# Kernel optimization log

Hardware: AMD Instinct MI355X
Metric: run time of the kernel (lower is better)

Reference implementation:

```python
import jax, jax.numpy as jnp
import numpy as np


def _lap(cost):
    """Jonker-Volgenant / e-maxx O(n^3) Hungarian (min-cost) on a square
    float64 cost matrix. Returns col index assigned to each row, matching
    scipy.optimize.linear_sum_assignment for square inputs.
    Inner column scan is vectorized with numpy.
    """
    n = cost.shape[0]
    INF = np.inf
    C = np.zeros((n + 1, n + 1), dtype=np.float64)
    C[1:, 1:] = cost  # 1-indexed
    u = np.zeros(n + 1)
    v = np.zeros(n + 1)
    p = np.zeros(n + 1, dtype=np.int64)    # p[j] = row matched to col j
    way = np.zeros(n + 1, dtype=np.int64)
    for i in range(1, n + 1):
        p[0] = i
        j0 = 0
        minv = np.full(n + 1, INF)
        used = np.zeros(n + 1, dtype=bool)
        while True:
            used[j0] = True
            i0 = p[j0]
            free = ~used
            free[0] = False
            cur = C[i0] - u[i0] - v
            upd = free & (cur < minv)
            minv = np.where(upd, cur, minv)
            way[upd] = j0
            mv = np.where(free, minv, INF)
            j1 = int(np.argmin(mv))
            delta = mv[j1]
            u[p[used]] += delta
            v[used] -= delta
            minv = np.where(free, minv - delta, minv)
            j0 = j1
            if p[j0] == 0:
                break
        # augment along alternating path
        while j0 != 0:
            j1 = way[j0]
            p[j0] = p[j1]
            j0 = j1
    col_for_row = np.zeros(n, dtype=np.int64)
    col_for_row[p[1:] - 1] = np.arange(n)
    return col_for_row


def _match(D_np):
    """Per-sample min-max normalize (detached) then Hungarian match."""
    B, N, _ = D_np.shape
    cols = np.zeros((B, N), dtype=np.int64)
    for b in range(B):
        Db = D_np[b]
        d_min = Db.min()
        d_range = Db.max() - d_min + 1e-8
        cols[b] = _lap((Db - d_min) / d_range)
    return cols


def setup_inputs() -> dict:
    key = jax.random.key(0)
    B, N = 32, 512
    D = jax.random.uniform(key, (B, N, N), dtype=jnp.float32)
    return {"D": D}


def reference(D):
    B, N, _ = D.shape
    # Matching indices are computed on detached, normalized costs (CPU, like
    # the original .cpu().numpy() round-trip).
    D_np = np.asarray(jax.device_get(D), dtype=np.float64)
    cols = jnp.asarray(_match(D_np))                      # [B, N]
    bi = jnp.arange(B)[:, None]
    ri = jnp.arange(N)[None, :]
    matched = D[bi, ri, cols]                             # [B, N], original D
    return matched.mean(axis=1).mean()
```

## Files before the change

### kernel.cpp

```cpp
#include <hip/hip_runtime.h>
#include <hip/hip_fp16.h>


#define NN 512
#define LPT 8
#define BIGF 1e30f
#define QCAP 2080
#define ARRCAP 1536

#define DPP_MINF(x, CTRL) do {                                                  \
    float _t = __int_as_float(__builtin_amdgcn_update_dpp(                      \
        __float_as_int(x), __float_as_int(x), CTRL, 0xf, 0xf, false));          \
    (x) = _t < (x) ? _t : (x);                                                  \
} while (0)

__device__ __forceinline__ float wave_min_f32(float x) {
    DPP_MINF(x, 0x111);
    DPP_MINF(x, 0x112);
    DPP_MINF(x, 0x114);
    DPP_MINF(x, 0x118);
    DPP_MINF(x, 0x142);
    DPP_MINF(x, 0x143);
    return __int_as_float(__builtin_amdgcn_readlane(__float_as_int(x), 63));
}

template <bool F16>
__global__ __launch_bounds__(64)
void hungarian_kernel(const float* __restrict__ D, const __half* __restrict__ Hm,
                      double* __restrict__ bsum) {
    const int b    = blockIdx.x;
    const int lane = threadIdx.x;
    const float*  __restrict__ Db = D + (size_t)b * NN * NN;
    const __half* __restrict__ Hb = F16 ? (Hm + (size_t)b * NN * NN) : (const __half*)nullptr;

    __shared__ int p[NN + 1];
    __shared__ int way[NN + 1];
    __shared__ int xrow[NN + 1];
    __shared__ int q[QCAP];
    __shared__ int qn[2];

    for (int k = lane; k <= NN; k += 64) { p[k] = 0; way[k] = 0; xrow[k] = 0; }
    __syncthreads();

    const int col0 = lane * LPT;

    auto loadrow = [&](int r, float rv[LPT]) {
        if constexpr (F16) {
            const uint4 qv = *(const uint4*)(Hb + (size_t)(r - 1) * NN + col0);
            __half2 h0 = *(__half2*)&qv.x, h1 = *(__half2*)&qv.y,
                    h2 = *(__half2*)&qv.z, h3 = *(__half2*)&qv.w;
            float2 f0 = __half22float2(h0), f1 = __half22float2(h1),
                   f2 = __half22float2(h2), f3 = __half22float2(h3);
            rv[0]=f0.x; rv[1]=f0.y; rv[2]=f1.x; rv[3]=f1.y;
            rv[4]=f2.x; rv[5]=f2.y; rv[6]=f3.x; rv[7]=f3.y;
        } else {
            const float4* rp = (const float4*)(Db + (size_t)(r - 1) * NN + col0);
            const float4 a = rp[0], c = rp[1];
            rv[0]=a.x; rv[1]=a.y; rv[2]=a.z; rv[3]=a.w;
            rv[4]=c.x; rv[5]=c.y; rv[6]=c.z; rv[7]=c.w;
        }
    };
    auto loadsc = [&](int r, int j) -> float {
        if constexpr (F16) return __half2float(Hb[(size_t)(r - 1) * NN + (j - 1)]);
        else               return Db[(size_t)(r - 1) * NN + (j - 1)];
    };

    float v[LPT];

    {
        float cmin[LPT]; int cidx[LPT];
        #pragma unroll
        for (int s = 0; s < LPT; ++s) { cmin[s] = BIGF; cidx[s] = 0; }
        for (int r = 1; r <= NN; ++r) {
            float rv[LPT]; loadrow(r, rv);
            #pragma unroll
            for (int s = 0; s < LPT; ++s) {
                if (rv[s] < cmin[s]) { cmin[s] = rv[s]; cidx[s] = r; }
            }
        }
        #pragma unroll
        for (int s = 0; s < LPT; ++s) { v[s] = cmin[s]; way[col0 + s + 1] = cidx[s]; }
        __syncthreads();
        if (lane == 0) {
            for (int j = NN; j >= 1; --j) {
                const int i = way[j];
                if (xrow[i] == 0) { xrow[i] = j; p[j] = i; }
            }
        }
        __syncthreads();
    }

    if (lane == 0) {
        int t = 0;
        for (int r = 1; r <= NN; ++r) if (xrow[r] == 0) q[t++] = r;
        qn[0] = t;
    }
    __syncthreads();
    {
        int tail = qn[0], head = 0, processed = 0;
        while (head < tail && processed < ARRCAP) {
            const int i = q[head]; ++head; ++processed;
            float rv[LPT]; loadrow(i, rv);
            float cur[LPT];
            #pragma unroll
            for (int s = 0; s < LPT; ++s) cur[s] = rv[s] - v[s];
            float b1 = BIGF; int bj = NN;
            #pragma unroll
            for (int s = 0; s < LPT; ++s) {
                if (cur[s] < b1) { b1 = cur[s]; bj = col0 + s + 1; }
            }
            const float u1 = wave_min_f32(b1);
            const unsigned long long m1 = __ballot(b1 == u1);
            const int owner = __ffsll(m1) - 1;
            const int j1    = __builtin_amdgcn_readlane(bj, owner);
            const int slotU = (j1 - 1) & 7;
            #pragma unroll
            for (int s = 0; s < LPT; ++s)
                if (lane == owner && s == slotU) cur[s] = BIGF;
            float b2 = BIGF;
            #pragma unroll
            for (int s = 0; s < LPT; ++s) b2 = cur[s] < b2 ? cur[s] : b2;
            const float u2 = wave_min_f32(b2);

            const int i1 = p[j1];
            const bool steal = (u1 < u2);
            if (steal && lane == owner) {
                #pragma unroll
                for (int s = 0; s < LPT; ++s) if (s == slotU) v[s] -= (u2 - u1);
            }
            if (i1 == 0) {
                if (lane == 0) { p[j1] = i; xrow[i] = j1; }
            } else if (steal && tail < QCAP - 1) {
                if (lane == 0) { p[j1] = i; xrow[i] = j1; xrow[i1] = 0; q[tail] = i1; }
                ++tail;
            }
            __syncthreads();
        }
    }
    __syncthreads();

    if (lane == 0) {
        int t = 0;
        for (int r = 1; r <= NN; ++r) if (xrow[r] == 0) q[t++] = r;
        qn[0] = t;
    }
    __syncthreads();
    const int nfree = qn[0];

    for (int fi = 0; fi < nfree; ++fi) {
        const int i = q[fi];
        if (lane == 0) p[0] = i;

        float minv[LPT]; int wayreg[LPT];
        #pragma unroll
        for (int s = 0; s < LPT; ++s) { minv[s] = BIGF; wayreg[s] = 0; }
        unsigned usedmask = 0;
        int   j0 = 0;
        float uu = 0.0f;

        float rv[LPT]; loadrow(i, rv);
        __syncthreads();

        float dfinal;
        while (true) {
            if (j0 > 0) {
                const int jc = j0 - 1;
                if ((jc >> 3) == lane) usedmask |= 1u << (jc & 7);
            }
            float bestv = BIGF; int bestj = NN;
            #pragma unroll
            for (int s = 0; s < LPT; ++s) {
                const bool freeS = !(usedmask & (1u << s));
                const float cur  = rv[s] - uu - v[s];
                const bool upd   = freeS && (cur < minv[s]);
                minv[s]   = upd ? cur : minv[s];
                wayreg[s] = upd ? j0  : wayreg[s];
                const bool better = freeS && (minv[s] < bestv);
                bestj = better ? (col0 + s + 1) : bestj;
                bestv = better ? minv[s] : bestv;
            }
            const float dmin = wave_min_f32(bestv);
            const unsigned long long mk = __ballot(bestv == dmin);
            const int owner = __ffsll(mk) - 1;
            const int j1    = __builtin_amdgcn_readlane(bestj, owner);

            const int i0n = p[j1];
            if (i0n == 0) { j0 = j1; dfinal = dmin; break; }

            const int slotU = (j1 - 1) & 7;
            float vs = v[0];
            #pragma unroll
            for (int s = 1; s < LPT; ++s) vs = (slotU == s) ? v[s] : vs;
            const float vj1 = __int_as_float(
                __builtin_amdgcn_readlane(__float_as_int(vs), owner));

            const float csc = loadsc(i0n, j1);
            loadrow(i0n, rv);
            uu = csc - vj1 - dmin;
            j0 = j1;
        }

        #pragma unroll
        for (int s = 0; s < LPT; ++s) {
            way[col0 + s + 1] = wayreg[s];
            if (usedmask & (1u << s)) v[s] += minv[s] - dfinal;
        }
        __syncthreads();
        if (lane == 0) {
            int jj = j0;
            while (jj != 0) { const int jp = way[jj]; p[jj] = p[jp]; jj = jp; }
        }
        __syncthreads();
    }

    double acc = 0.0;
    #pragma unroll
    for (int s = 0; s < LPT; ++s) {
        const int j = col0 + s + 1;
        const int r = p[j] - 1;
        acc += (double)Db[(size_t)r * NN + (j - 1)];
    }
    #pragma unroll
    for (int m = 1; m < 64; m <<= 1) acc += __shfl_xor(acc, m, 64);
    if (lane == 0) bsum[b] = acc;
}

__global__ void cvt_kernel(const float* __restrict__ D, __half* __restrict__ H, int n4) {
    const int idx = blockIdx.x * blockDim.x + threadIdx.x;
    const int stride = gridDim.x * blockDim.x;
    const float4* __restrict__ D4 = (const float4*)D;
    __half2* __restrict__ H2 = (__half2*)H;
    for (int i = idx; i < n4; i += stride) {
        const float4 f = D4[i];
        H2[2 * i]     = __floats2half2_rn(f.x, f.y);
        H2[2 * i + 1] = __floats2half2_rn(f.z, f.w);
    }
}

__global__ void finalize_kernel(const double* __restrict__ bsum, float* __restrict__ out, int B) {
    if (threadIdx.x == 0 && blockIdx.x == 0) {
        double acc = 0.0;
        for (int b = 0; b < B; ++b) acc += bsum[b] / (double)NN;
        out[0] = (float)(acc / (double)B);
    }
}

extern "C" void kernel_launch(void* const* d_in, const int* in_sizes, int n_in,
                              void* d_out, int out_size, void* d_ws, size_t ws_size,
                              hipStream_t stream) {
    (void)n_in; (void)out_size;
    const float* D    = (const float*)d_in[0];
    float*       out  = (float*)d_out;
    double*      bsum = (double*)d_ws;

    const int B = in_sizes[0] / (NN * NN);
    const size_t need = 256 + (size_t)B * NN * NN * sizeof(__half);

    if (ws_size >= need) {
        __half* Hm = (__half*)((char*)d_ws + 256);
        const int n4 = (B * NN * NN) / 4;
        cvt_kernel<<<1024, 256, 0, stream>>>(D, Hm, n4);
        hungarian_kernel<true><<<dim3(B), dim3(64), 0, stream>>>(D, Hm, bsum);
    } else {
        hungarian_kernel<false><<<dim3(B), dim3(64), 0, stream>>>(D, nullptr, bsum);
    }
    finalize_kernel<<<1, 64, 0, stream>>>(bsum, out, B);
}
```

Baseline: 2.956 ms.

## Keep assignment in registers, add reduction-transfer pass, replace barriers with wave barriers

Mirrors the column-to-row assignment array into per-lane registers so the augmenting loops read it via readlane instead of shared memory. Adds a JV reduction-transfer pass before the auction-style augmenting row reduction. Replaces the used bitmask with an additive blocking array and precomputed row-minus-v values, and uses tree argmin helpers. Swaps __syncthreads for wave barriers since the block is a single wave. The extra pass adds work and changes the heuristic's path, which could alter the number of Dijkstra searches.

```diff
diff --git a/kernel.cpp b/kernel.cpp
--- a/kernel.cpp
+++ b/kernel.cpp
@@ -24,6 +24,30 @@
     return __int_as_float(__builtin_amdgcn_readlane(__float_as_int(x), 63));
 }
 
+__device__ __forceinline__ void wavebar() { __builtin_amdgcn_wave_barrier(); }
+
+__device__ __forceinline__ int sel8i(const int a[LPT], int slot) {
+    int r = a[0];
+    #pragma unroll
+    for (int s = 1; s < LPT; ++s) r = (slot == s) ? a[s] : r;
+    return r;
+}
+__device__ __forceinline__ float sel8f(const float a[LPT], int slot) {
+    float r = a[0];
+    #pragma unroll
+    for (int s = 1; s < LPT; ++s) r = (slot == s) ? a[s] : r;
+    return r;
+}
+__device__ __forceinline__ void argmin8(const float e[LPT], float& bv, int& bs) {
+    float v01 = e[1] < e[0] ? e[1] : e[0]; int s01 = e[1] < e[0] ? 1 : 0;
+    float v23 = e[3] < e[2] ? e[3] : e[2]; int s23 = e[3] < e[2] ? 3 : 2;
+    float v45 = e[5] < e[4] ? e[5] : e[4]; int s45 = e[5] < e[4] ? 5 : 4;
+    float v67 = e[7] < e[6] ? e[7] : e[6]; int s67 = e[7] < e[6] ? 7 : 6;
+    float v03 = v23 < v01 ? v23 : v01;     int s03 = v23 < v01 ? s23 : s01;
+    float v47 = v67 < v45 ? v67 : v45;     int s47 = v67 < v45 ? s67 : s45;
+    bv = v47 < v03 ? v47 : v03;            bs = v47 < v03 ? s47 : s03;
+}
+
 template <bool F16>
 __global__ __launch_bounds__(64)
 void hungarian_kernel(const float* __restrict__ D, const __half* __restrict__ Hm,
@@ -33,14 +57,14 @@
     const float*  __restrict__ Db = D + (size_t)b * NN * NN;
     const __half* __restrict__ Hb = F16 ? (Hm + (size_t)b * NN * NN) : (const __half*)nullptr;
 
-    __shared__ int p[NN + 1];
-    __shared__ int way[NN + 1];
-    __shared__ int xrow[NN + 1];
+    __shared__ __align__(16) int pc[NN];
+    __shared__ __align__(16) int wayc[NN];
+    __shared__ __align__(16) int xrowc[NN];
     __shared__ int q[QCAP];
-    __shared__ int qn[2];
-
-    for (int k = lane; k <= NN; k += 64) { p[k] = 0; way[k] = 0; xrow[k] = 0; }
-    __syncthreads();
+    __shared__ int qn;
+
+    for (int k = lane; k < NN; k += 64) { pc[k] = 0; wayc[k] = 0; xrowc[k] = 0; }
+    wavebar();
 
     const int col0 = lane * LPT;
 
@@ -66,159 +90,201 @@
     };
 
     float v[LPT];
+    int   preg[LPT];
 
     {
         float cmin[LPT]; int cidx[LPT];
         #pragma unroll
         for (int s = 0; s < LPT; ++s) { cmin[s] = BIGF; cidx[s] = 0; }
+        #pragma unroll 4
         for (int r = 1; r <= NN; ++r) {
             float rv[LPT]; loadrow(r, rv);
             #pragma unroll
             for (int s = 0; s < LPT; ++s) {
-                if (rv[s] < cmin[s]) { cmin[s] = rv[s]; cidx[s] = r; }
-            }
-        }
-        #pragma unroll
-        for (int s = 0; s < LPT; ++s) { v[s] = cmin[s]; way[col0 + s + 1] = cidx[s]; }
-        __syncthreads();
+                const bool c = rv[s] < cmin[s];
+                cidx[s] = c ? r : cidx[s];
+                cmin[s] = c ? rv[s] : cmin[s];
+            }
+        }
+        #pragma unroll
+        for (int s = 0; s < LPT; ++s) v[s] = cmin[s];
+        *(int4*)&wayc[col0]     = make_int4(cidx[0], cidx[1], cidx[2], cidx[3]);
+        *(int4*)&wayc[col0 + 4] = make_int4(cidx[4], cidx[5], cidx[6], cidx[7]);
+        wavebar();
         if (lane == 0) {
             for (int j = NN; j >= 1; --j) {
-                const int i = way[j];
-                if (xrow[i] == 0) { xrow[i] = j; p[j] = i; }
-            }
-        }
-        __syncthreads();
+                const int i = wayc[j - 1];
+                if (xrowc[i - 1] == 0) { xrowc[i - 1] = j; pc[j - 1] = i; }
+            }
+        }
+        wavebar();
+        const int4 p0 = *(const int4*)&pc[col0];
+        const int4 p1 = *(const int4*)&pc[col0 + 4];
+        preg[0]=p0.x; preg[1]=p0.y; preg[2]=p0.z; preg[3]=p0.w;
+        preg[4]=p1.x; preg[5]=p1.y; preg[6]=p1.z; preg[7]=p1.w;
+    }
+
+    int xr[LPT];
+    {
+        const int4 x0 = *(const int4*)&xrowc[col0];
+        const int4 x1 = *(const int4*)&xrowc[col0 + 4];
+        xr[0]=x0.x; xr[1]=x0.y; xr[2]=x0.z; xr[3]=x0.w;
+        xr[4]=x1.x; xr[5]=x1.y; xr[6]=x1.z; xr[7]=x1.w;
+    }
+
+    for (int i = 1; i <= NN; ++i) {
+        const int jx = __builtin_amdgcn_readlane(sel8i(xr, (i - 1) & 7), (i - 1) >> 3);
+        if (jx == 0) continue;
+        float rv[LPT]; loadrow(i, rv);
+        const int  ow = (jx - 1) >> 3, sl = (jx - 1) & 7;
+        const bool am = (lane == ow);
+        float lm = BIGF;
+        #pragma unroll
+        for (int s = 0; s < LPT; ++s) {
+            const float t = (am && s == sl) ? BIGF : (rv[s] - v[s]);
+            lm = t < lm ? t : lm;
+        }
+        const float mu = wave_min_f32(lm);
+        #pragma unroll
+        for (int s = 0; s < LPT; ++s)
+            if (am && s == sl) v[s] = rv[s] - mu;
     }
 
     if (lane == 0) {
         int t = 0;
-        for (int r = 1; r <= NN; ++r) if (xrow[r] == 0) q[t++] = r;
-        qn[0] = t;
-    }
-    __syncthreads();
+        for (int r = 1; r <= NN; ++r) if (xrowc[r - 1] == 0) q[t++] = r;
+        qn = t;
+    }
+    wavebar();
     {
-        int tail = qn[0], head = 0, processed = 0;
+        int tail = qn, head = 0, processed = 0;
         while (head < tail && processed < ARRCAP) {
             const int i = q[head]; ++head; ++processed;
             float rv[LPT]; loadrow(i, rv);
             float cur[LPT];
             #pragma unroll
             for (int s = 0; s < LPT; ++s) cur[s] = rv[s] - v[s];
-            float b1 = BIGF; int bj = NN;
-            #pragma unroll
-            for (int s = 0; s < LPT; ++s) {
-                if (cur[s] < b1) { b1 = cur[s]; bj = col0 + s + 1; }
-            }
+            float b1; int bs1; argmin8(cur, b1, bs1);
             const float u1 = wave_min_f32(b1);
             const unsigned long long m1 = __ballot(b1 == u1);
             const int owner = __ffsll(m1) - 1;
-            const int j1    = __builtin_amdgcn_readlane(bj, owner);
+            const int j1    = __builtin_amdgcn_readlane(col0 + bs1 + 1, owner);
             const int slotU = (j1 - 1) & 7;
+            const bool am   = (lane == owner);
             #pragma unroll
             for (int s = 0; s < LPT; ++s)
-                if (lane == owner && s == slotU) cur[s] = BIGF;
+                if (am && s == slotU) cur[s] = BIGF;
             float b2 = BIGF;
             #pragma unroll
             for (int s = 0; s < LPT; ++s) b2 = cur[s] < b2 ? cur[s] : b2;
             const float u2 = wave_min_f32(b2);
-
-            const int i1 = p[j1];
-            const bool steal = (u1 < u2);
-            if (steal && lane == owner) {
+            const int  i1  = __builtin_amdgcn_readlane(sel8i(preg, slotU), owner);
+            const bool steal  = (u1 < u2);
+            const bool assign = (i1 == 0) || (steal && (tail < QCAP - 1));
+            if (assign) {
                 #pragma unroll
-                for (int s = 0; s < LPT; ++s) if (s == slotU) v[s] -= (u2 - u1);
-            }
-            if (i1 == 0) {
-                if (lane == 0) { p[j1] = i; xrow[i] = j1; }
-            } else if (steal && tail < QCAP - 1) {
-                if (lane == 0) { p[j1] = i; xrow[i] = j1; xrow[i1] = 0; q[tail] = i1; }
-                ++tail;
-            }
-            __syncthreads();
-        }
-    }
-    __syncthreads();
+                for (int s = 0; s < LPT; ++s) {
+                    if (am && s == slotU) {
+                        if (steal) v[s] -= (u2 - u1);
+                        preg[s] = i;
+                    }
+                }
+                if (lane == 0) {
+                    pc[j1 - 1] = i; xrowc[i - 1] = j1;
+                    if (i1) { xrowc[i1 - 1] = 0; q[tail] = i1; }
+                }
+                if (i1) ++tail;
+            }
+            wavebar();
+        }
+    }
+    wavebar();
 
     if (lane == 0) {
         int t = 0;
-        for (int r = 1; r <= NN; ++r) if (xrow[r] == 0) q[t++] = r;
-        qn[0] = t;
-    }
-    __syncthreads();
-    const int nfree = qn[0];
+        for (int r = 1; r <= NN; ++r) if (xrowc[r - 1] == 0) q[t++] = r;
+        qn = t;
+    }
+    wavebar();
+    const int nfree = qn;
 
     for (int fi = 0; fi < nfree; ++fi) {
-        const int i = q[fi];
-        if (lane == 0) p[0] = i;
-
-        float minv[LPT]; int wayreg[LPT];
-        #pragma unroll
-        for (int s = 0; s < LPT; ++s) { minv[s] = BIGF; wayreg[s] = 0; }
-        unsigned usedmask = 0;
+        const int rootI = q[fi];
+
+        float minv[LPT], blk[LPT], w[LPT];
+        int   wayreg[LPT];
+        #pragma unroll
+        for (int s = 0; s < LPT; ++s) { minv[s] = BIGF; blk[s] = 0.0f; wayreg[s] = 0; }
+        float uu = 0.0f;
         int   j0 = 0;
-        float uu = 0.0f;
-
-        float rv[LPT]; loadrow(i, rv);
-        __syncthreads();
-
-        float dfinal;
+
+        float rv[LPT]; loadrow(rootI, rv);
+        #pragma unroll
+        for (int s = 0; s < LPT; ++s) w[s] = rv[s] - v[s];
+
+        int j1; float dmin;
         while (true) {
-            if (j0 > 0) {
-                const int jc = j0 - 1;
-                if ((jc >> 3) == lane) usedmask |= 1u << (jc & 7);
-            }
-            float bestv = BIGF; int bestj = NN;
             #pragma unroll
             for (int s = 0; s < LPT; ++s) {
-                const bool freeS = !(usedmask & (1u << s));
-                const float cur  = rv[s] - uu - v[s];
-                const bool upd   = freeS && (cur < minv[s]);
-                minv[s]   = upd ? cur : minv[s];
-                wayreg[s] = upd ? j0  : wayreg[s];
-                const bool better = freeS && (minv[s] < bestv);
-                bestj = better ? (col0 + s + 1) : bestj;
-                bestv = better ? minv[s] : bestv;
-            }
-            const float dmin = wave_min_f32(bestv);
-            const unsigned long long mk = __ballot(bestv == dmin);
+                const float c  = (w[s] - uu) + blk[s];
+                const bool upd = c < minv[s];
+                wayreg[s] = upd ? j0 : wayreg[s];
+                minv[s]   = upd ? c  : minv[s];
+            }
+            float e[LPT];
+            #pragma unroll
+            for (int s = 0; s < LPT; ++s) e[s] = minv[s] + blk[s];
+            float bv; int bs; argmin8(e, bv, bs);
+            dmin = wave_min_f32(bv);
+            const unsigned long long mk = __ballot(bv == dmin);
             const int owner = __ffsll(mk) - 1;
-            const int j1    = __builtin_amdgcn_readlane(bestj, owner);
-
-            const int i0n = p[j1];
-            if (i0n == 0) { j0 = j1; dfinal = dmin; break; }
-
+            j1 = __builtin_amdgcn_readlane(col0 + bs + 1, owner);
             const int slotU = (j1 - 1) & 7;
-            float vs = v[0];
-            #pragma unroll
-            for (int s = 1; s < LPT; ++s) vs = (slotU == s) ? v[s] : vs;
-            const float vj1 = __int_as_float(
-                __builtin_amdgcn_readlane(__float_as_int(vs), owner));
+            const int i0n   = __builtin_amdgcn_readlane(sel8i(preg, slotU), owner);
+            if (i0n == 0) break;
 
             const float csc = loadsc(i0n, j1);
             loadrow(i0n, rv);
+            const float vj1 = __int_as_float(__builtin_amdgcn_readlane(
+                __float_as_int(sel8f(v, slotU)), owner));
+            const bool am = (lane == owner);
+            #pragma unroll
+            for (int s = 0; s < LPT; ++s)
+                if (am && s == slotU) blk[s] = BIGF;
             uu = csc - vj1 - dmin;
+            #pragma unroll
+            for (int s = 0; s < LPT; ++s) w[s] = rv[s] - v[s];
             j0 = j1;
         }
-
-        #pragma unroll
-        for (int s = 0; s < LPT; ++s) {
-            way[col0 + s + 1] = wayreg[s];
-            if (usedmask & (1u << s)) v[s] += minv[s] - dfinal;
-        }
-        __syncthreads();
+        const float dfinal = dmin;
+        j0 = j1;
+
+        #pragma unroll
+        for (int s = 0; s < LPT; ++s)
+            if (blk[s] == BIGF) v[s] += minv[s] - dfinal;
+        *(int4*)&wayc[col0]     = make_int4(wayreg[0], wayreg[1], wayreg[2], wayreg[3]);
+        *(int4*)&wayc[col0 + 4] = make_int4(wayreg[4], wayreg[5], wayreg[6], wayreg[7]);
+        wavebar();
         if (lane == 0) {
             int jj = j0;
-            while (jj != 0) { const int jp = way[jj]; p[jj] = p[jp]; jj = jp; }
-        }
-        __syncthreads();
+            while (jj != 0) {
+                const int jp = wayc[jj - 1];
+                pc[jj - 1] = jp ? pc[jp - 1] : rootI;
+                jj = jp;
+            }
+        }
+        wavebar();
+        const int4 p0 = *(const int4*)&pc[col0];
+        const int4 p1 = *(const int4*)&pc[col0 + 4];
+        preg[0]=p0.x; preg[1]=p0.y; preg[2]=p0.z; preg[3]=p0.w;
+        preg[4]=p1.x; preg[5]=p1.y; preg[6]=p1.z; preg[7]=p1.w;
     }
 
     double acc = 0.0;
     #pragma unroll
     for (int s = 0; s < LPT; ++s) {
-        const int j = col0 + s + 1;
-        const int r = p[j] - 1;
-        acc += (double)Db[(size_t)r * NN + (j - 1)];
+        const int r = preg[s];
+        acc += (double)Db[(size_t)(r - 1) * NN + (col0 + s)];
     }
     #pragma unroll
     for (int m = 1; m < 64; m <<= 1) acc += __shfl_xor(acc, m, 64);
```

Measured after the change: 2.925 ms. About the same (-1.1%).
